# Kernel optimization log

Measured on AMD Instinct MI355X. Metric: run time of the kernel, lower is better.

## Reference

```python
import jax, jax.numpy as jnp
import numpy as np

B, EMBED, HEADS, T = 2, 512, 8, 2048
DH = EMBED // HEADS
EPS = 1e-5
# NOTE: torch code computes embed_dim // num_heads ** 0.5 == 512 // sqrt(8)
SCALE = EMBED // HEADS ** 0.5  # = 181.0, reproduced faithfully


def ws_conv1x1(x, w, b, mask):
    # weight-standardized 1x1 conv; w: [O, I], x: [B, I, T], mask: [B, T]
    mu = jnp.mean(w, axis=1, keepdims=True)
    var = jnp.var(w, axis=1, keepdims=True)
    wn = (w - mu) * jax.lax.rsqrt(var + EPS)
    x = x * mask[:, None, :].astype(x.dtype)
    return jnp.einsum('oi,bit->bot', wn, x) + b[None, :, None]


def ln_head(x, g, b):
    # per-head LayerNorm over head dim; x: [B, H, DH, T], normalized over DH
    xt = jnp.swapaxes(x, -1, -2)  # [B, H, T, DH]
    mu = jnp.mean(xt, axis=-1, keepdims=True)
    var = jnp.var(xt, axis=-1, keepdims=True)
    xn = (xt - mu) * jax.lax.rsqrt(var + EPS) * g + b
    return jnp.swapaxes(xn, -1, -2)


def setup_inputs():
    key = jax.random.key(0)
    ks = jax.random.split(key, 12)
    sc = 1.0 / np.sqrt(EMBED)
    d = {
        'q': jax.random.normal(ks[0], (B, EMBED, T), jnp.float32),
        'k': jax.random.normal(ks[1], (B, EMBED, T), jnp.float32),
        'v': jax.random.normal(ks[2], (B, EMBED, T), jnp.float32),
        'query_mask': jax.random.randint(ks[3], (B, T), 0, 2, jnp.int32),
        'key_mask': jax.random.randint(ks[4], (B, T), 0, 2, jnp.int32),
        'value_mask': jax.random.randint(ks[5], (B, T), 0, 2, jnp.int32),
        'Wq': jax.random.normal(ks[6], (EMBED, EMBED), jnp.float32) * sc,
        'bq': jnp.zeros((EMBED,), jnp.float32),
        'Wk': jax.random.normal(ks[7], (EMBED, EMBED), jnp.float32) * sc,
        'bk': jnp.zeros((EMBED,), jnp.float32),
        'Wv': jax.random.normal(ks[8], (EMBED, EMBED), jnp.float32) * sc,
        'bv': jnp.zeros((EMBED,), jnp.float32),
        'Wo': jax.random.normal(ks[9], (EMBED, EMBED), jnp.float32) * sc,
        'bo': jnp.zeros((EMBED,), jnp.float32),
        'ln_gq': jnp.ones((DH,), jnp.float32), 'ln_bq': jnp.zeros((DH,), jnp.float32),
        'ln_gk': jnp.ones((DH,), jnp.float32), 'ln_bk': jnp.zeros((DH,), jnp.float32),
        'ln_gv': jnp.ones((DH,), jnp.float32), 'ln_bv': jnp.zeros((DH,), jnp.float32),
    }
    return d


def reference(q, k, v, query_mask, key_mask, value_mask,
              Wq, bq, Wk, bk, Wv, bv, Wo, bo,
              ln_gq, ln_bq, ln_gk, ln_bk, ln_gv, ln_bv):
    q = ws_conv1x1(q, Wq, bq, query_mask)   # [B, E, T]
    k = ws_conv1x1(k, Wk, bk, key_mask)
    v = ws_conv1x1(v, Wv, bv, value_mask)
    # split heads: [B, E, T] -> [B, H, DH, T]
    q = q.reshape(B, HEADS, DH, T)
    k = k.reshape(B, HEADS, DH, T)
    v = v.reshape(B, HEADS, DH, T)
    # middle_norm: per-head LayerNorm over DH
    q = ln_head(q, ln_gq, ln_bq)
    k = ln_head(k, ln_gk, ln_bk)
    v = ln_head(v, ln_gv, ln_bv)
    # scores = q^T k / scale : [B, H, Tq, Tk]
    scores = jnp.einsum('bhdq,bhdk->bhqk', q, k) / SCALE
    scores = jnp.where(key_mask[:, None, None, :] == 0, -1e9, scores)
    scores = jax.nn.softmax(scores, axis=-1)
    scores = jnp.where(query_mask[:, None, :, None] == 0, 0.0, scores)
    # out = (scores @ v^T)^T : [B, H, DH, Tq]
    out = jnp.einsum('bhqk,bhdk->bhdq', scores, v)
    out = out.reshape(B, EMBED, T)
    out = ws_conv1x1(out, Wo, bo, query_mask)
    return out
```

## Files before the change

### kernel.cpp

```cpp
#include <hip/hip_runtime.h>


typedef __bf16 bf16;
typedef __bf16 bf16x2 __attribute__((ext_vector_type(2)));
typedef __bf16 bf16x8 __attribute__((ext_vector_type(8)));
typedef _Float16 f16;
typedef _Float16 f16x8 __attribute__((ext_vector_type(8)));
typedef float  f32x4  __attribute__((ext_vector_type(4)));

#define MFMA_BF16(a, b, c) __builtin_amdgcn_mfma_f32_16x16x32_bf16((a), (b), (c), 0, 0, 0)
#define MFMA_F16_K32(a, b, c) __builtin_amdgcn_mfma_f32_16x16x32_f16((a), (b), (c), 0, 0, 0)

#if __has_builtin(__builtin_amdgcn_exp2f)
#define EXP2F(x) __builtin_amdgcn_exp2f(x)
#else
#define EXP2F(x) __expf((x) * 0.6931471805599453f)
#endif

#define NB   2
#define NE   512
#define NH   8
#define NT   2048
#define NDH  64
#define VF_BH_STRIDE (64 * 5 * 64 * 8)

__device__ __forceinline__ void gl_lds16(const bf16* g, bf16* l) {
  __builtin_amdgcn_global_load_lds(
      (const __attribute__((address_space(1))) void*)g,
      (__attribute__((address_space(3))) void*)l, 16, 0, 0);
}

__global__ __launch_bounds__(64) void k_wstd(
    const float* __restrict__ Wq, const float* __restrict__ Wk,
    const float* __restrict__ Wv, const float* __restrict__ Wo,
    bf16* __restrict__ out)
{
  const float* W = blockIdx.y == 0 ? Wq : blockIdx.y == 1 ? Wk
                 : blockIdx.y == 2 ? Wv : Wo;
  int row = blockIdx.x, lane = threadIdx.x;
  const float4* p = (const float4*)(W + row * NE) + lane * 2;
  float4 a = p[0], c = p[1];
  float s  = a.x + a.y + a.z + a.w + c.x + c.y + c.z + c.w;
  float ss = a.x*a.x + a.y*a.y + a.z*a.z + a.w*a.w
           + c.x*c.x + c.y*c.y + c.z*c.z + c.w*c.w;
#pragma unroll
  for (int m = 1; m < 64; m <<= 1) { s += __shfl_xor(s, m); ss += __shfl_xor(ss, m); }
  float mean = s * (1.0f / NE);
  float var  = ss * (1.0f / NE) - mean * mean;
  float rstd = rsqrtf(var + 1e-5f);
  bf16x8 o;
  o[0] = (bf16)((a.x - mean) * rstd); o[1] = (bf16)((a.y - mean) * rstd);
  o[2] = (bf16)((a.z - mean) * rstd); o[3] = (bf16)((a.w - mean) * rstd);
  o[4] = (bf16)((c.x - mean) * rstd); o[5] = (bf16)((c.y - mean) * rstd);
  o[6] = (bf16)((c.z - mean) * rstd); o[7] = (bf16)((c.w - mean) * rstd);
  *(bf16x8*)(out + blockIdx.y * (NE * NE) + row * NE + lane * 8) = o;
}

__global__ __launch_bounds__(256) void k_trans(
    const float* __restrict__ q, const float* __restrict__ k,
    const float* __restrict__ v,
    const int* __restrict__ qm, const int* __restrict__ km,
    const int* __restrict__ vm,
    bf16* __restrict__ xT)
{
  int src = blockIdx.z >> 1, b = blockIdx.z & 1;
  const float* x = src == 0 ? q : src == 1 ? k : v;
  const int*   m = src == 0 ? qm : src == 1 ? km : vm;
  x += (size_t)b * NE * NT;
  m += b * NT;
  int t0 = blockIdx.x * 64, i0 = blockIdx.y * 64;
  __shared__ float tile[64][65];
  int lr = threadIdx.x >> 4;
  int tc = (threadIdx.x & 15) * 4;
#pragma unroll
  for (int p = 0; p < 4; p++) {
    int row = p * 16 + lr;
    float4 v4 = *(const float4*)(x + (size_t)(i0 + row) * NT + t0 + tc);
    tile[row][tc]     = v4.x; tile[row][tc + 1] = v4.y;
    tile[row][tc + 2] = v4.z; tile[row][tc + 3] = v4.w;
  }
  __syncthreads();
  bf16* o = xT + ((size_t)src * NB + b) * NT * NE;
  int i2 = (threadIdx.x & 31) * 2, t2 = threadIdx.x >> 5;
#pragma unroll
  for (int t = t2; t < 64; t += 8) {
    float mk = (float)m[t0 + t];
    bf16x2 w2;
    w2[0] = (bf16)(tile[i2][t] * mk);
    w2[1] = (bf16)(tile[i2 + 1][t] * mk);
    *(bf16x2*)(o + (size_t)(t0 + t) * NE + i0 + i2) = w2;
  }
}

__global__ __launch_bounds__(256) void k_proj(
    const bf16* __restrict__ Wn,
    const bf16* __restrict__ xT,
    const int* __restrict__ km,
    const float* __restrict__ bq, const float* __restrict__ bk,
    const float* __restrict__ bv,
    const float* __restrict__ gq, const float* __restrict__ bbq,
    const float* __restrict__ gk, const float* __restrict__ bbk,
    const float* __restrict__ gv, const float* __restrict__ bbv,
    bf16* __restrict__ Qh, bf16* __restrict__ Kh, f16* __restrict__ Vf)
{
  int src = blockIdx.z >> 1, b = blockIdx.z & 1;
  const bf16* A  = Wn + src * (NE * NE);
  const bf16* Bm = xT + ((size_t)src * NB + b) * NT * NE;
  int m0 = blockIdx.y * 64, n0 = blockIdx.x * 128;
  int h = m0 >> 6;

  __shared__ __align__(16) char smem[64 * 130 * 4 + 2 * 128 * 4];
  bf16*  Al = (bf16*)smem;
  bf16*  Bl = (bf16*)(smem + 8192);
  float* Yl = (float*)smem;
  float* mu = (float*)(smem + 64 * 130 * 4);
  float* rs = mu + 128;

  int tid = threadIdx.x, lane = tid & 63, w = tid >> 6;
  int mh = (w & 1) * 32, nh = (w >> 1) * 64;
  f32x4 acc[2][4] = {};

  for (int k0 = 0; k0 < NE; k0 += 64) {
    __syncthreads();
#pragma unroll
    for (int i = 0; i < 2; i++) {
      int row = (w << 4) + (i << 3) + (lane >> 3);
      int chg = (lane & 7) ^ (row & 7);
      gl_lds16(A + (m0 + row) * NE + k0 + (chg << 3),
               Al + ((w << 4) + (i << 3)) * 64);
    }
#pragma unroll
    for (int i = 0; i < 4; i++) {
      int row = (w << 5) + (i << 3) + (lane >> 3);
      int chg = (lane & 7) ^ (row & 7);
      gl_lds16(Bm + (size_t)(n0 + row) * NE + k0 + (chg << 3),
               Bl + ((w << 5) + (i << 3)) * 64);
    }
    __syncthreads();
#pragma unroll
    for (int kk = 0; kk < 64; kk += 32) {
      bf16x8 af[2], bfv[4];
#pragma unroll
      for (int ms = 0; ms < 2; ms++) {
        int row = mh + ms * 16 + (lane & 15);
        af[ms] = *(const bf16x8*)(Al + row * 64 +
                   ((((kk >> 3) + (lane >> 4)) ^ (row & 7)) << 3));
      }
#pragma unroll
      for (int ns = 0; ns < 4; ns++) {
        int row = nh + ns * 16 + (lane & 15);
        bfv[ns] = *(const bf16x8*)(Bl + row * 64 +
                   ((((kk >> 3) + (lane >> 4)) ^ (row & 7)) << 3));
      }
#pragma unroll
      for (int ms = 0; ms < 2; ms++)
#pragma unroll
        for (int ns = 0; ns < 4; ns++)
          acc[ms][ns] = MFMA_BF16(af[ms], bfv[ns], acc[ms][ns]);
    }
  }

  __syncthreads();
  {
    const float* bias = src == 0 ? bq : src == 1 ? bk : bv;
#pragma unroll
    for (int ms = 0; ms < 2; ms++)
#pragma unroll
      for (int ns = 0; ns < 4; ns++)
#pragma unroll
        for (int r = 0; r < 4; r++) {
          int om = mh + ms * 16 + ((lane >> 4) << 2) + r;
          int on = nh + ns * 16 + (lane & 15);
          Yl[om * 130 + on] = acc[ms][ns][r] + bias[m0 + om];
        }
  }
  __syncthreads();
  if (tid < 128) {
    float s = 0.f, ss = 0.f;
#pragma unroll 8
    for (int o = 0; o < 64; o++) { float y = Yl[o * 130 + tid]; s += y; ss += y * y; }
    float mean = s * (1.0f / 64.0f);
    float var  = ss * (1.0f / 64.0f) - mean * mean;
    mu[tid] = mean;
    rs[tid] = rsqrtf(var + 1e-5f);
  }
  __syncthreads();

  if (src < 2) {
    float scl = (src == 0) ? (1.4426950408889634f / 181.0f) : 1.0f;
    const float* g  = src == 0 ? gq  : gk;
    const float* bb = src == 0 ? bbq : bbk;
    bf16* out = (src == 0 ? Qh : Kh) + ((size_t)(b * NH + h) * NT + n0) * NDH;
    int d = tid & 63, tb = tid >> 6;
    float gg = g[d] * scl, bb2 = bb[d] * scl;
#pragma unroll
    for (int t = tb; t < 128; t += 4) {
      float val = (Yl[d * 130 + t] - mu[t]) * rs[t] * gg + bb2;
      out[(size_t)t * NDH + d] = (bf16)val;
    }
  } else {
    int gl = tid >> 6, lane2 = tid & 63;
    int quad2 = lane2 >> 4, l15b = lane2 & 15;
    int bh = b * NH + h;
    f16* base = Vf + (size_t)bh * VF_BH_STRIDE
              + (size_t)((n0 >> 5) + gl) * (5 * 64 * 8) + lane2 * 8;
    int   tl[8]; float mk[8];
#pragma unroll
    for (int j = 0; j < 8; j++) {
      tl[j] = gl * 32 + ((j < 4) ? quad2 * 4 + j : 16 + quad2 * 4 + (j - 4));
      mk[j] = (float)km[b * NT + n0 + tl[j]];
    }
#pragma unroll
    for (int ds = 0; ds < 4; ds++) {
      int d = ds * 16 + l15b;
      float gg = gv[d], bb3 = bbv[d];
      f16x8 o;
#pragma unroll
      for (int j = 0; j < 8; j++) {
        int t = tl[j];
        o[j] = (f16)(((Yl[d * 130 + t] - mu[t]) * rs[t] * gg + bb3) * mk[j]);
      }
      *(f16x8*)(base + ds * (64 * 8)) = o;
    }
    f16x8 om;
#pragma unroll
    for (int j = 0; j < 8; j++) om[j] = (f16)mk[j];
    *(f16x8*)(base + 4 * (64 * 8)) = om;
  }
}

__global__ __launch_bounds__(256) void k_attn(
    const bf16* __restrict__ Qh, const bf16* __restrict__ Kh,
    const f16* __restrict__ Vf, const int* __restrict__ qmask,
    bf16* __restrict__ xa)
{
  int bh = blockIdx.y, b = bh >> 3, h = bh & 7;
  int q0 = blockIdx.x * 64;
  const bf16* Q = Qh + (size_t)bh * NT * NDH;
  const bf16* K = Kh + (size_t)bh * NT * NDH;
  const f16*  VfB = Vf + (size_t)bh * VF_BH_STRIDE;

  __shared__ __align__(16) char smem[2 * 64 * 68 * 4 + 4 * 64 * 4];
  float* OlA  = (float*)smem;
  float* OlB  = (float*)(smem + 64 * 68 * 4);
  float* denl = (float*)(smem + 2 * 64 * 68 * 4);

  int tid = threadIdx.x, lane = tid & 63, w = tid >> 6;
  int quad = lane >> 4, l15 = lane & 15;
  const int ko = w * 32;

  bf16x8 qb[4][2];
#pragma unroll
  for (int qs = 0; qs < 4; qs++)
#pragma unroll
    for (int hf = 0; hf < 2; hf++)
      qb[qs][hf] = *(const bf16x8*)(Q + (size_t)(q0 + qs * 16 + l15) * NDH + hf * 32 + quad * 8);

  const bf16* Kb = K + (size_t)(ko + l15) * NDH + quad * 8;

  f32x4 acco[4][4] = {};
  f32x4 dacc[4]    = {};

  bf16x8 ka[2][2];
  f16x8  vb8[5];
#pragma unroll
  for (int kt = 0; kt < 2; kt++)
#pragma unroll
    for (int hf = 0; hf < 2; hf++)
      ka[kt][hf] = *(const bf16x8*)(Kb + (size_t)(kt * 16) * NDH + hf * 32);
#pragma unroll
  for (int j5 = 0; j5 < 5; j5++)
    vb8[j5] = *(const f16x8*)(VfB + ((size_t)w * 5 + j5) * 512 + lane * 8);

  for (int k0 = 0; k0 < NT; k0 += 128) {
    int k1 = (k0 + 128) & (NT - 1);
    int g1 = (k1 >> 5) + w;
    bf16x8 nka[2][2];
    f16x8  nvb[5];
#pragma unroll
    for (int kt = 0; kt < 2; kt++)
#pragma unroll
      for (int hf = 0; hf < 2; hf++)
        nka[kt][hf] = *(const bf16x8*)(Kb + (size_t)(k1 + kt * 16) * NDH + hf * 32);
#pragma unroll
    for (int j5 = 0; j5 < 5; j5++)
      nvb[j5] = *(const f16x8*)(VfB + ((size_t)g1 * 5 + j5) * 512 + lane * 8);

#pragma unroll
    for (int qs = 0; qs < 4; qs++) {
      f32x4 z0 = {}, z1 = {};
      z0 = MFMA_BF16(ka[0][0], qb[qs][0], z0);
      z0 = MFMA_BF16(ka[0][1], qb[qs][1], z0);
      z1 = MFMA_BF16(ka[1][0], qb[qs][0], z1);
      z1 = MFMA_BF16(ka[1][1], qb[qs][1], z1);
      f16x8 pa;
#pragma unroll
      for (int r = 0; r < 4; r++) {
        pa[r]     = (f16)EXP2F(z0[r]);
        pa[4 + r] = (f16)EXP2F(z1[r]);
      }
      dacc[qs] = MFMA_F16_K32(pa, vb8[4], dacc[qs]);
#pragma unroll
      for (int ds = 0; ds < 4; ds++)
        acco[qs][ds] = MFMA_F16_K32(pa, vb8[ds], acco[qs][ds]);
    }

#pragma unroll
    for (int kt = 0; kt < 2; kt++)
#pragma unroll
      for (int hf = 0; hf < 2; hf++)
        ka[kt][hf] = nka[kt][hf];
#pragma unroll
    for (int j5 = 0; j5 < 5; j5++)
      vb8[j5] = nvb[j5];
  }

  if (l15 == 0)
#pragma unroll
    for (int qs = 0; qs < 4; qs++)
#pragma unroll
      for (int r = 0; r < 4; r++)
        denl[w * 64 + qs * 16 + quad * 4 + r] = dacc[qs][r];

  float* Obuf = (w < 2) ? OlA : OlB;
  if ((w & 1) == 0) {
#pragma unroll
    for (int qs = 0; qs < 4; qs++)
#pragma unroll
      for (int ds = 0; ds < 4; ds++)
#pragma unroll
        for (int r = 0; r < 4; r++)
          Obuf[(qs * 16 + quad * 4 + r) * 68 + ds * 16 + l15] = acco[qs][ds][r];
  }
  __syncthreads();
  if (w & 1) {
#pragma unroll
    for (int qs = 0; qs < 4; qs++)
#pragma unroll
      for (int ds = 0; ds < 4; ds++)
#pragma unroll
        for (int r = 0; r < 4; r++)
          Obuf[(qs * 16 + quad * 4 + r) * 68 + ds * 16 + l15] += acco[qs][ds][r];
  }
  __syncthreads();

#pragma unroll
  for (int i = 0; i < 16; i++) {
    int ql = w * 16 + i;
    float dtot = denl[ql] + denl[64 + ql] + denl[128 + ql] + denl[192 + ql];
    float qm = (float)qmask[b * NT + q0 + ql];
    float inv = qm / dtot;
    float val = (OlA[ql * 68 + lane] + OlB[ql * 68 + lane]) * inv;
    xa[((size_t)b * NT + q0 + ql) * NE + h * NDH + lane] = (bf16)val;
  }
}

__global__ __launch_bounds__(256) void k_oproj(
    const bf16* __restrict__ A,
    const bf16* __restrict__ xab,
    const float* __restrict__ bo, float* __restrict__ out)
{
  int b = blockIdx.z;
  const bf16* Bm = xab + (size_t)b * NT * NE;
  int m0 = blockIdx.y * 64, n0 = blockIdx.x * 64;

  __shared__ __align__(16) char smem[16384];
  bf16* Al = (bf16*)smem;
  bf16* Bl = (bf16*)(smem + 8192);

  int tid = threadIdx.x, lane = tid & 63, w = tid >> 6;
  int mh = (w & 1) * 32, nh = (w >> 1) * 32;
  f32x4 acc[2][2] = {};

  for (int k0 = 0; k0 < NE; k0 += 64) {
    __syncthreads();
#pragma unroll
    for (int i = 0; i < 2; i++) {
      int row = (w << 4) + (i << 3) + (lane >> 3);
      int chg = (lane & 7) ^ (row & 7);
      gl_lds16(A + (m0 + row) * NE + k0 + (chg << 3),
               Al + ((w << 4) + (i << 3)) * 64);
    }
#pragma unroll
    for (int i = 0; i < 2; i++) {
      int row = (w << 4) + (i << 3) + (lane >> 3);
      int chg = (lane & 7) ^ (row & 7);
      gl_lds16(Bm + (size_t)(n0 + row) * NE + k0 + (chg << 3),
               Bl + ((w << 4) + (i << 3)) * 64);
    }
    __syncthreads();
#pragma unroll
    for (int kk = 0; kk < 64; kk += 32) {
      bf16x8 af[2], bfv[2];
#pragma unroll
      for (int ms = 0; ms < 2; ms++) {
        int row = mh + ms * 16 + (lane & 15);
        af[ms] = *(const bf16x8*)(Al + row * 64 +
                   ((((kk >> 3) + (lane >> 4)) ^ (row & 7)) << 3));
      }
#pragma unroll
      for (int ns = 0; ns < 2; ns++) {
        int row = nh + ns * 16 + (lane & 15);
        bfv[ns] = *(const bf16x8*)(Bl + row * 64 +
                   ((((kk >> 3) + (lane >> 4)) ^ (row & 7)) << 3));
      }
#pragma unroll
      for (int ms = 0; ms < 2; ms++)
#pragma unroll
        for (int ns = 0; ns < 2; ns++)
          acc[ms][ns] = MFMA_BF16(af[ms], bfv[ns], acc[ms][ns]);
    }
  }

#pragma unroll
  for (int ms = 0; ms < 2; ms++)
#pragma unroll
    for (int ns = 0; ns < 2; ns++)
#pragma unroll
      for (int r = 0; r < 4; r++) {
        int o = m0 + mh + ms * 16 + ((lane >> 4) << 2) + r;
        int t = n0 + nh + ns * 16 + (lane & 15);
        out[(size_t)b * NE * NT + (size_t)o * NT + t] = acc[ms][ns][r] + bo[o];
      }
}

extern "C" void kernel_launch(void* const* d_in, const int* in_sizes, int n_in,
                              void* d_out, int out_size, void* d_ws, size_t ws_size,
                              hipStream_t stream)
{
  const float* q  = (const float*)d_in[0];
  const float* k  = (const float*)d_in[1];
  const float* v  = (const float*)d_in[2];
  const int*   qm = (const int*)d_in[3];
  const int*   km = (const int*)d_in[4];
  const int*   vm = (const int*)d_in[5];
  const float* Wq = (const float*)d_in[6];  const float* bq = (const float*)d_in[7];
  const float* Wk = (const float*)d_in[8];  const float* bk = (const float*)d_in[9];
  const float* Wv = (const float*)d_in[10]; const float* bv = (const float*)d_in[11];
  const float* Wo = (const float*)d_in[12]; const float* bo = (const float*)d_in[13];
  const float* gq = (const float*)d_in[14]; const float* bbq = (const float*)d_in[15];
  const float* gk = (const float*)d_in[16]; const float* bbk = (const float*)d_in[17];
  const float* gv = (const float*)d_in[18]; const float* bbv = (const float*)d_in[19];
  float* out = (float*)d_out;

  char* wsb = (char*)d_ws;
  bf16*  Wn  = (bf16*)(wsb);
  bf16*  xT  = (bf16*)(wsb + (2ull  << 20));
  bf16*  xa  = (bf16*)(wsb + (2ull  << 20));
  bf16*  Qh  = (bf16*)(wsb + (14ull << 20));
  bf16*  Kh  = (bf16*)(wsb + (18ull << 20));
  f16*   Vf  = (f16*) (wsb + (22ull << 20));

  k_wstd <<<dim3(512, 4),   64,  0, stream>>>(Wq, Wk, Wv, Wo, Wn);
  k_trans<<<dim3(32, 8, 6), 256, 0, stream>>>(q, k, v, qm, km, vm, xT);
  k_proj <<<dim3(16, 8, 6), 256, 0, stream>>>(Wn, xT, km, bq, bk, bv,
                                              gq, bbq, gk, bbk, gv, bbv,
                                              Qh, Kh, Vf);
  k_attn <<<dim3(32, 16),   256, 0, stream>>>(Qh, Kh, Vf, qm, xa);
  k_oproj<<<dim3(32, 8, 2), 256, 0, stream>>>(Wn + 3 * NE * NE, xa, bo, out);
}
```

Baseline: 170.9 us.

## Widen GEMM K-tiles to 128, unroll attention with two-stage KV prefetch, pack Q/K stores

The projection and output GEMMs now stage 128-wide K slices in LDS with a 16-way XOR swizzle, which halves the number of barrier-separated iterations at the cost of more LDS per block. The attention kernel's KV loop is fully unrolled with two register stages, each prefetched one step ahead, to hide global load latency better, though it raises register pressure. The Q/K epilogue writes two bf16 values per store to cut store instruction count.

```diff
diff --git a/kernel.cpp b/kernel.cpp
--- a/kernel.cpp
+++ b/kernel.cpp
@@ -109,48 +109,47 @@
   int m0 = blockIdx.y * 64, n0 = blockIdx.x * 128;
   int h = m0 >> 6;
 
-  __shared__ __align__(16) char smem[64 * 130 * 4 + 2 * 128 * 4];
+  __shared__ __align__(16) char smem[49152];
   bf16*  Al = (bf16*)smem;
-  bf16*  Bl = (bf16*)(smem + 8192);
+  bf16*  Bl = (bf16*)(smem + 16384);
   float* Yl = (float*)smem;
   float* mu = (float*)(smem + 64 * 130 * 4);
   float* rs = mu + 128;
 
   int tid = threadIdx.x, lane = tid & 63, w = tid >> 6;
   int mh = (w & 1) * 32, nh = (w >> 1) * 64;
+  int lr4 = lane >> 4, c16 = lane & 15;
   f32x4 acc[2][4] = {};
 
-  for (int k0 = 0; k0 < NE; k0 += 64) {
+  for (int k0 = 0; k0 < NE; k0 += 128) {
     __syncthreads();
 #pragma unroll
-    for (int i = 0; i < 2; i++) {
-      int row = (w << 4) + (i << 3) + (lane >> 3);
-      int chg = (lane & 7) ^ (row & 7);
-      gl_lds16(A + (m0 + row) * NE + k0 + (chg << 3),
-               Al + ((w << 4) + (i << 3)) * 64);
-    }
-#pragma unroll
     for (int i = 0; i < 4; i++) {
-      int row = (w << 5) + (i << 3) + (lane >> 3);
-      int chg = (lane & 7) ^ (row & 7);
-      gl_lds16(Bm + (size_t)(n0 + row) * NE + k0 + (chg << 3),
-               Bl + ((w << 5) + (i << 3)) * 64);
+      int row = w * 16 + i * 4 + lr4;
+      gl_lds16(A + (m0 + row) * NE + k0 + ((c16 ^ (row & 15)) << 3),
+               Al + (w * 16 + i * 4) * 128);
+    }
+#pragma unroll
+    for (int i = 0; i < 8; i++) {
+      int row = w * 32 + i * 4 + lr4;
+      gl_lds16(Bm + (size_t)(n0 + row) * NE + k0 + ((c16 ^ (row & 15)) << 3),
+               Bl + (w * 32 + i * 4) * 128);
     }
     __syncthreads();
 #pragma unroll
-    for (int kk = 0; kk < 64; kk += 32) {
+    for (int kk = 0; kk < 128; kk += 32) {
       bf16x8 af[2], bfv[4];
 #pragma unroll
       for (int ms = 0; ms < 2; ms++) {
         int row = mh + ms * 16 + (lane & 15);
-        af[ms] = *(const bf16x8*)(Al + row * 64 +
-                   ((((kk >> 3) + (lane >> 4)) ^ (row & 7)) << 3));
+        int slot = ((kk >> 3) + (lane >> 4)) ^ (row & 15);
+        af[ms] = *(const bf16x8*)(Al + row * 128 + (slot << 3));
       }
 #pragma unroll
       for (int ns = 0; ns < 4; ns++) {
         int row = nh + ns * 16 + (lane & 15);
-        bfv[ns] = *(const bf16x8*)(Bl + row * 64 +
-                   ((((kk >> 3) + (lane >> 4)) ^ (row & 7)) << 3));
+        int slot = ((kk >> 3) + (lane >> 4)) ^ (row & 15);
+        bfv[ns] = *(const bf16x8*)(Bl + row * 128 + (slot << 3));
       }
 #pragma unroll
       for (int ms = 0; ms < 2; ms++)
@@ -191,12 +190,16 @@
     const float* g  = src == 0 ? gq  : gk;
     const float* bb = src == 0 ? bbq : bbk;
     bf16* out = (src == 0 ? Qh : Kh) + ((size_t)(b * NH + h) * NT + n0) * NDH;
-    int d = tid & 63, tb = tid >> 6;
-    float gg = g[d] * scl, bb2 = bb[d] * scl;
-#pragma unroll
-    for (int t = tb; t < 128; t += 4) {
-      float val = (Yl[d * 130 + t] - mu[t]) * rs[t] * gg + bb2;
-      out[(size_t)t * NDH + d] = (bf16)val;
+    int d2 = (tid & 31) * 2, tb2 = tid >> 5;
+    float g0 = g[d2] * scl,     b0 = bb[d2] * scl;
+    float g1 = g[d2 + 1] * scl, b1 = bb[d2 + 1] * scl;
+#pragma unroll
+    for (int t = tb2; t < 128; t += 8) {
+      float rmu = mu[t], rrs = rs[t];
+      bf16x2 w2;
+      w2[0] = (bf16)((Yl[d2 * 130 + t] - rmu) * rrs * g0 + b0);
+      w2[1] = (bf16)((Yl[(d2 + 1) * 130 + t] - rmu) * rrs * g1 + b1);
+      *(bf16x2*)(out + (size_t)t * NDH + d2) = w2;
     }
   } else {
     int gl = tid >> 6, lane2 = tid & 63;
@@ -229,6 +232,46 @@
   }
 }
 
+struct KV {
+  bf16x8 ka[2][2];
+  f16x8  vb[5];
+};
+
+__device__ __forceinline__ void kv_load(KV& s, const bf16* Kb, const f16* VfW,
+                                        int kk) {
+#pragma unroll
+  for (int kt = 0; kt < 2; kt++)
+#pragma unroll
+    for (int hf = 0; hf < 2; hf++)
+      s.ka[kt][hf] = *(const bf16x8*)(Kb + (size_t)(kk + kt * 16) * NDH + hf * 32);
+  const f16* vp = VfW + (size_t)(kk >> 5) * (5 * 512);
+#pragma unroll
+  for (int j5 = 0; j5 < 5; j5++)
+    s.vb[j5] = *(const f16x8*)(vp + j5 * 512);
+}
+
+__device__ __forceinline__ void kv_comp(const KV& s, const bf16x8 qb[4][2],
+                                        f32x4 acco[4][4], f32x4 dacc[4]) {
+#pragma unroll
+  for (int qs = 0; qs < 4; qs++) {
+    f32x4 z0 = {}, z1 = {};
+    z0 = MFMA_BF16(s.ka[0][0], qb[qs][0], z0);
+    z0 = MFMA_BF16(s.ka[0][1], qb[qs][1], z0);
+    z1 = MFMA_BF16(s.ka[1][0], qb[qs][0], z1);
+    z1 = MFMA_BF16(s.ka[1][1], qb[qs][1], z1);
+    f16x8 pa;
+#pragma unroll
+    for (int r = 0; r < 4; r++) {
+      pa[r]     = (f16)EXP2F(z0[r]);
+      pa[4 + r] = (f16)EXP2F(z1[r]);
+    }
+    dacc[qs] = MFMA_F16_K32(pa, s.vb[4], dacc[qs]);
+#pragma unroll
+    for (int ds = 0; ds < 4; ds++)
+      acco[qs][ds] = MFMA_F16_K32(pa, s.vb[ds], acco[qs][ds]);
+  }
+}
+
 __global__ __launch_bounds__(256) void k_attn(
     const bf16* __restrict__ Qh, const bf16* __restrict__ Kh,
     const f16* __restrict__ Vf, const int* __restrict__ qmask,
@@ -256,63 +299,24 @@
     for (int hf = 0; hf < 2; hf++)
       qb[qs][hf] = *(const bf16x8*)(Q + (size_t)(q0 + qs * 16 + l15) * NDH + hf * 32 + quad * 8);
 
-  const bf16* Kb = K + (size_t)(ko + l15) * NDH + quad * 8;
+  const bf16* Kb  = K + (size_t)(ko + l15) * NDH + quad * 8;
+  const f16*  VfW = VfB + (size_t)w * (5 * 512) + lane * 8;
 
   f32x4 acco[4][4] = {};
   f32x4 dacc[4]    = {};
 
-  bf16x8 ka[2][2];
-  f16x8  vb8[5];
-#pragma unroll
-  for (int kt = 0; kt < 2; kt++)
-#pragma unroll
-    for (int hf = 0; hf < 2; hf++)
-      ka[kt][hf] = *(const bf16x8*)(Kb + (size_t)(kt * 16) * NDH + hf * 32);
-#pragma unroll
-  for (int j5 = 0; j5 < 5; j5++)
-    vb8[j5] = *(const f16x8*)(VfB + ((size_t)w * 5 + j5) * 512 + lane * 8);
-
-  for (int k0 = 0; k0 < NT; k0 += 128) {
-    int k1 = (k0 + 128) & (NT - 1);
-    int g1 = (k1 >> 5) + w;
-    bf16x8 nka[2][2];
-    f16x8  nvb[5];
-#pragma unroll
-    for (int kt = 0; kt < 2; kt++)
-#pragma unroll
-      for (int hf = 0; hf < 2; hf++)
-        nka[kt][hf] = *(const bf16x8*)(Kb + (size_t)(k1 + kt * 16) * NDH + hf * 32);
-#pragma unroll
-    for (int j5 = 0; j5 < 5; j5++)
-      nvb[j5] = *(const f16x8*)(VfB + ((size_t)g1 * 5 + j5) * 512 + lane * 8);
-
-#pragma unroll
-    for (int qs = 0; qs < 4; qs++) {
-      f32x4 z0 = {}, z1 = {};
-      z0 = MFMA_BF16(ka[0][0], qb[qs][0], z0);
-      z0 = MFMA_BF16(ka[0][1], qb[qs][1], z0);
-      z1 = MFMA_BF16(ka[1][0], qb[qs][0], z1);
-      z1 = MFMA_BF16(ka[1][1], qb[qs][1], z1);
-      f16x8 pa;
-#pragma unroll
-      for (int r = 0; r < 4; r++) {
-        pa[r]     = (f16)EXP2F(z0[r]);
-        pa[4 + r] = (f16)EXP2F(z1[r]);
-      }
-      dacc[qs] = MFMA_F16_K32(pa, vb8[4], dacc[qs]);
-#pragma unroll
-      for (int ds = 0; ds < 4; ds++)
-        acco[qs][ds] = MFMA_F16_K32(pa, vb8[ds], acco[qs][ds]);
-    }
-
-#pragma unroll
-    for (int kt = 0; kt < 2; kt++)
-#pragma unroll
-      for (int hf = 0; hf < 2; hf++)
-        ka[kt][hf] = nka[kt][hf];
-#pragma unroll
-    for (int j5 = 0; j5 < 5; j5++)
-      vb8[j5] = nvb[j5];
+  KV s0, s1;
+  kv_load(s0, Kb, VfW, 0);
+  kv_load(s1, Kb, VfW, 128);
+
+#pragma unroll
+  for (int i = 0; i < 8; i++) {
+    KV n0, n1;
+    if (i < 7) kv_load(n0, Kb, VfW, i * 256 + 256);
+    kv_comp(s0, qb, acco, dacc);
+    if (i < 7) kv_load(n1, Kb, VfW, i * 256 + 384);
+    kv_comp(s1, qb, acco, dacc);
+    if (i < 7) { s0 = n0; s1 = n1; }
   }
 
   if (l15 == 0)
@@ -364,45 +368,44 @@
   const bf16* Bm = xab + (size_t)b * NT * NE;
   int m0 = blockIdx.y * 64, n0 = blockIdx.x * 64;
 
-  __shared__ __align__(16) char smem[16384];
+  __shared__ __align__(16) char smem[32768];
   bf16* Al = (bf16*)smem;
-  bf16* Bl = (bf16*)(smem + 8192);
+  bf16* Bl = (bf16*)(smem + 16384);
 
   int tid = threadIdx.x, lane = tid & 63, w = tid >> 6;
   int mh = (w & 1) * 32, nh = (w >> 1) * 32;
+  int lr4 = lane >> 4, c16 = lane & 15;
   f32x4 acc[2][2] = {};
 
-  for (int k0 = 0; k0 < NE; k0 += 64) {
+  for (int k0 = 0; k0 < NE; k0 += 128) {
     __syncthreads();
 #pragma unroll
-    for (int i = 0; i < 2; i++) {
-      int row = (w << 4) + (i << 3) + (lane >> 3);
-      int chg = (lane & 7) ^ (row & 7);
-      gl_lds16(A + (m0 + row) * NE + k0 + (chg << 3),
-               Al + ((w << 4) + (i << 3)) * 64);
-    }
-#pragma unroll
-    for (int i = 0; i < 2; i++) {
-      int row = (w << 4) + (i << 3) + (lane >> 3);
-      int chg = (lane & 7) ^ (row & 7);
-      gl_lds16(Bm + (size_t)(n0 + row) * NE + k0 + (chg << 3),
-               Bl + ((w << 4) + (i << 3)) * 64);
+    for (int i = 0; i < 4; i++) {
+      int row = w * 16 + i * 4 + lr4;
+      gl_lds16(A + (m0 + row) * NE + k0 + ((c16 ^ (row & 15)) << 3),
+               Al + (w * 16 + i * 4) * 128);
+    }
+#pragma unroll
+    for (int i = 0; i < 4; i++) {
+      int row = w * 16 + i * 4 + lr4;
+      gl_lds16(Bm + (size_t)(n0 + row) * NE + k0 + ((c16 ^ (row & 15)) << 3),
+               Bl + (w * 16 + i * 4) * 128);
     }
     __syncthreads();
 #pragma unroll
-    for (int kk = 0; kk < 64; kk += 32) {
+    for (int kk = 0; kk < 128; kk += 32) {
       bf16x8 af[2], bfv[2];
 #pragma unroll
       for (int ms = 0; ms < 2; ms++) {
         int row = mh + ms * 16 + (lane & 15);
-        af[ms] = *(const bf16x8*)(Al + row * 64 +
-                   ((((kk >> 3) + (lane >> 4)) ^ (row & 7)) << 3));
+        int slot = ((kk >> 3) + (lane >> 4)) ^ (row & 15);
+        af[ms] = *(const bf16x8*)(Al + row * 128 + (slot << 3));
       }
 #pragma unroll
       for (int ns = 0; ns < 2; ns++) {
         int row = nh + ns * 16 + (lane & 15);
-        bfv[ns] = *(const bf16x8*)(Bl + row * 64 +
-                   ((((kk >> 3) + (lane >> 4)) ^ (row & 7)) << 3));
+        int slot = ((kk >> 3) + (lane >> 4)) ^ (row & 15);
+        bfv[ns] = *(const bf16x8*)(Bl + row * 128 + (slot << 3));
       }
 #pragma unroll
       for (int ms = 0; ms < 2; ms++)
```

After: 156.6 us. 1.09x faster.
